# Kernel tuning notes

Measured on AMD Instinct MI355X. Metric: run time of the kernel, lower is better.

Reference implementation:

```python
import jax, jax.numpy as jnp
import numpy as np

H_HEADS = 8
TOP_K = 32


def _interp_matrix(n_out, n_in):
    # 1D linear-interp matrix matching torch trilinear, align_corners=False
    c = (jnp.arange(n_out, dtype=jnp.float32) + 0.5) * (n_in / n_out) - 0.5
    c = jnp.clip(c, 0.0, n_in - 1)
    i0 = jnp.floor(c).astype(jnp.int32)
    i1 = jnp.minimum(i0 + 1, n_in - 1)
    w = c - i0.astype(jnp.float32)
    r = jnp.arange(n_out)
    Mt = jnp.zeros((n_out, n_in), jnp.float32)
    return Mt.at[r, i0].add(1.0 - w).at[r, i1].add(w)


def _ln(x, g, b, eps=1e-5):
    m = x.mean(axis=-1, keepdims=True)
    v = ((x - m) ** 2).mean(axis=-1, keepdims=True)
    return (x - m) * jax.lax.rsqrt(v + eps) * g + b


def _forward(x, mask, pe, Wqkv, bqkv, Wo, bo, ln1_g, ln1_b, W1, b1, W2, b2,
             ln2_g, ln2_b, gate, mem_k, mem_v, fc1_w, fc1_b, fc2_w, fc2_b):
    B, D = x.shape[0], x.shape[1]
    H, HD, K = H_HEADS, D // H_HEADS, TOP_K
    # FeatureConcatenator treated as identity (x already concatenated features)
    Im = _interp_matrix(8, mask.shape[2])  # separable trilinear resize 64->8
    m8 = jnp.einsum('ai,bj,ck,nqijk->nqabc', Im, Im, Im, mask)
    h = x * m8 + pe  # masked features + learned absolute 3D positional enc
    tok = h.reshape(B, D, -1).transpose(0, 2, 1)  # [B, S=512, D]
    scale = 1.0 / jnp.sqrt(jnp.float32(HD))
    L = Wqkv.shape[0]
    for l in range(L):
        qkv = tok @ Wqkv[l] + bqkv[l]
        q, k, v = jnp.split(qkv, 3, axis=-1)
        hd = lambda t: t.reshape(B, -1, H, HD).transpose(0, 2, 1, 3)  # [B,H,S,d]
        q, k, v = hd(q), hd(k), hd(v)
        attn = jax.nn.softmax(jnp.einsum('bhsd,bhtd->bhst', q, k) * scale, axis=-1)
        out = jnp.einsum('bhst,bhtd->bhsd', attn, v)
        if l == 0:  # KNN memory layer: irregular top-k retrieval over memory bank
            sim = jnp.einsum('bhsd,bmd->bhsm', q, mem_k) * scale  # [B,H,S,M]
            top_sim, top_idx = jax.lax.top_k(sim, K)  # [B,H,S,K]
            mv = jnp.take_along_axis(mem_v[:, None, None], top_idx[..., None], axis=3)
            mem_out = jnp.einsum('bhsk,bhskd->bhsd', jax.nn.softmax(top_sim, axis=-1), mv)
            g = jax.nn.sigmoid(gate)[None, :, None, None]
            out = out * (1.0 - g) + mem_out * g
        out = out.transpose(0, 2, 1, 3).reshape(B, -1, D)
        tok = _ln(tok + out @ Wo[l] + bo[l], ln1_g[l], ln1_b[l])
        ff = jax.nn.gelu(tok @ W1[l] + b1[l], approximate=False) @ W2[l] + b2[l]
        tok = _ln(tok + ff, ln2_g[l], ln2_b[l])
    pooled = tok.mean(axis=1)  # global avg pool over all 512 voxels
    return jax.nn.gelu(pooled @ fc1_w + fc1_b, approximate=False) @ fc2_w + fc2_b


def setup_inputs() -> dict:
    key = jax.random.key(0)
    ks = jax.random.split(key, 24)
    B, D, Sp, M, L = 4, 512, 8, 8192, 6
    H, HD, FF, MLP, NC = 8, 64, 2048, 1024, 117
    nrm = lambda k, shp, s=0.02: jax.random.normal(k, shp, jnp.float32) * s
    return {
        'x': jax.random.normal(ks[0], (B, D, Sp, Sp, Sp), jnp.float32),
        'mask': jax.random.uniform(ks[1], (B, 1, 64, 64, 64), jnp.float32),
        'pe': nrm(ks[2], (1, D, Sp, Sp, Sp)),
        'Wqkv': nrm(ks[3], (L, D, 3 * D)),
        'bqkv': jnp.zeros((L, 3 * D), jnp.float32),
        'Wo': nrm(ks[4], (L, D, D)),
        'bo': jnp.zeros((L, D), jnp.float32),
        'ln1_g': jnp.ones((L, D), jnp.float32),
        'ln1_b': jnp.zeros((L, D), jnp.float32),
        'W1': nrm(ks[5], (L, D, FF)),
        'b1': jnp.zeros((L, FF), jnp.float32),
        'W2': nrm(ks[6], (L, FF, D)),
        'b2': jnp.zeros((L, D), jnp.float32),
        'ln2_g': jnp.ones((L, D), jnp.float32),
        'ln2_b': jnp.zeros((L, D), jnp.float32),
        'gate': jnp.zeros((H,), jnp.float32),
        'mem_k': jax.random.normal(ks[7], (B, M, HD), jnp.float32),
        'mem_v': jax.random.normal(ks[8], (B, M, HD), jnp.float32),
        'fc1_w': nrm(ks[9], (D, MLP)),
        'fc1_b': jnp.zeros((MLP,), jnp.float32),
        'fc2_w': nrm(ks[10], (MLP, NC)),
        'fc2_b': jnp.zeros((NC,), jnp.float32),
    }


def reference(x, mask, pe, Wqkv, bqkv, Wo, bo, ln1_g, ln1_b, W1, b1, W2, b2,
              ln2_g, ln2_b, gate, mem_k, mem_v, fc1_w, fc1_b, fc2_w, fc2_b):
    return _forward(x, mask, pe, Wqkv, bqkv, Wo, bo, ln1_g, ln1_b, W1, b1, W2,
                    b2, ln2_g, ln2_b, gate, mem_k, mem_v, fc1_w, fc1_b, fc2_w, fc2_b)
```

## Files before the change

kernel.cpp:

```cpp
#include <hip/hip_runtime.h>
#include <hip/hip_bf16.h>
#include <float.h>
#include <math.h>

#define NB 4
#define ND 512
#define NS 512
#define NH 8
#define NHD 64
#define NM 8192
#define NL 6
#define NFF 2048
#define NMLP 1024
#define NC 117

#define KCC 64
#define NCC (NM / KCC)
#define CAPB 160
#define TRIG 96

#define CAPS 352
#define TRIGS 96

#define AS1 __attribute__((address_space(1)))
// ... 515 lines not shown
            }
#pragma unroll
            for (int fm = 0; fm < FM; ++fm)
#pragma unroll
                for (int fn = 0; fn < FN; ++fn) {
                    acc[fm][fn] = __builtin_amdgcn_mfma_f32_16x16x32_bf16(fah[fm], fbh[fn], acc[fm][fn], 0, 0, 0);
                    acc[fm][fn] = __builtin_amdgcn_mfma_f32_16x16x32_bf16(fah[fm], fbl[fn], acc[fm][fn], 0, 0, 0);
                    acc[fm][fn] = __builtin_amdgcn_mfma_f32_16x16x32_bf16(fal[fm], fbh[fn], acc[fm][fn], 0, 0, 0);
                }
        }
    }
#pragma unroll
    for (int fm = 0; fm < FM; ++fm) {
#pragma unroll
        for (int fn = 0; fn < FN; ++fn) {
            int n = bn + wc * (BN / 2) + fn * 16 + (lane & 15);
            float bb = 0.f;
            if (EPI != 3) bb = bias[n];
#pragma unroll
            for (int r = 0; r < 4; ++r) {
                int m = bm + wr * (BM / 2) + fm * 16 + (lane >> 4) * 4 + r;
                float o = acc[fm][fn][r] + bb;
                if (EPI == 4) {
                    o = gelu_f(o);
                    ushort hh, ll;
                    split1(o, hh, ll);
                    size_t byb = (size_t)m * 2 * N + (size_t)(n >> 6) * 128 +
                                 (size_t)(((((n >> 3) & 7) * 16)) ^ ((m & 7) << 4)) + (n & 7) * 2;
                    *(ushort*)((char*)CH + byb) = hh;
                    *(ushort*)((char*)CL + byb) = ll;
                } else if (EPI == 5) {
                    int seg = n >> 9;
                    int hh_ = (n >> 6) & 7, dd = n & 63;
                    int bq = m >> 9, sq = m & 511;
                    ushort hh, ll;
                    if (seg == 0) {
                        split1(o * 0.125f, hh, ll);
                        size_t rr = (size_t)bq * 4096 + hh_ * 512 + sq;
                        size_t by = rr * 128 + (size_t)((((dd >> 3) * 16)) ^ ((sq & 7) << 4)) + (dd & 7) * 2;
                        *(ushort*)((char*)CH + by) = hh;
                        *(ushort*)((char*)CL + by) = ll;
                    } else if (seg == 1) {
                        split1(o, hh, ll);
                        size_t rr = (size_t)bq * 4096 + hh_ * 512 + sq;
                        size_t by = rr * 128 + (size_t)((((dd >> 3) * 16)) ^ ((sq & 7) << 4)) + (dd & 7) * 2;
                        *(ushort*)((char*)C2H + by) = hh;
                        *(ushort*)((char*)C2L + by) = ll;
                    } else {
                        split1(o, hh, ll);
                        size_t rr = (size_t)(bq * 8 + hh_) * 64 + dd;
                        size_t by = rr * 1024 + (size_t)(sq >> 6) * 128 +
                                    (size_t)(((((sq >> 3) & 7) * 16)) ^ ((dd & 7) << 4)) + (sq & 7) * 2;
                        *(ushort*)((char*)C3H + by) = hh;
                        *(ushort*)((char*)C3L + by) = ll;
                    }
                } else {
                    if (EPI == 1) o = gelu_f(o);
                    else if (EPI == 2) o += resid[(size_t)m * N + n];
                    C[(size_t)m * N + n] = o;
                }
            }
        }
    }
}

__global__ __launch_bounds__(256) void k_attn2(
    const ushort* __restrict__ QH, const ushort* __restrict__ QL,
    const ushort* __restrict__ KH, const ushort* __restrict__ KL,
    const ushort* __restrict__ VTH, const ushort* __restrict__ VTL,
    float* __restrict__ ao) {
    __shared__ __align__(16) char SM[81920];
    int qt = blockIdx.x, h = blockIdx.y, b = blockIdx.z;
    int tid = threadIdx.x, lane = tid & 63, wvi = tid >> 6;
    size_t R = ((size_t)(b * NH + h)) * NS;
    const char* KHg = (const char*)KH + R * 128;
    const char* KLg = (const char*)KL + R * 128;
    const char* VHg = (const char*)VTH + ((size_t)(b * NH + h) * 64) * 1024;
    const char* VLg = (const char*)VTL + ((size_t)(b * NH + h) * 64) * 1024;

    stage_lin((const char*)QH + (R + qt * 64) * 128, SM + 65536, wvi, lane);
    stage_lin((const char*)QL + (R + qt * 64) * 128, SM + 73728, wvi, lane);
    stage_lin(KHg, SM + 0, wvi, lane);
    stage_lin(KLg, SM + 8192, wvi, lane);
    stage_vt(VHg, 0, SM + 32768, wvi, lane);
    stage_vt(VLg, 0, SM + 40960, wvi, lane);
    __syncthreads();

    s16x8 fqh[2], fql[2];
#pragma unroll
    for (int ks = 0; ks < 2; ++ks) {
        int row = wvi * 16 + (lane & 15);
        int by = row * 128 + ((((ks * 32 + (lane >> 4) * 8) * 2)) ^ ((row & 7) << 4));
        fqh[ks] = *(const s16x8*)(SM + 65536 + by);
        fql[ks] = *(const s16x8*)(SM + 73728 + by);
    }

    float mr_[4] = {-FLT_MAX, -FLT_MAX, -FLT_MAX, -FLT_MAX};
    float lr_[4] = {0.f, 0.f, 0.f, 0.f};
    f32x4 acc_o[4] = {};

    for (int c = 0; c < 8; ++c) {
        const char* khc = SM + ((c & 1) ? 16384 : 0);
        const char* klc = khc + 8192;
        const char* vhc = SM + 32768 + ((c & 1) ? 16384 : 0);
        const char* vlc = vhc + 8192;
        if (c + 1 < 8) {
            char* khn = SM + ((c & 1) ? 0 : 16384);
            char* vhn = SM + 32768 + ((c & 1) ? 0 : 16384);
            stage_lin(KHg + (size_t)(c + 1) * 8192, khn, wvi, lane);
            stage_lin(KLg + (size_t)(c + 1) * 8192, khn + 8192, wvi, lane);
            stage_vt(VHg, (c + 1) * 128, vhn, wvi, lane);
            stage_vt(VLg, (c + 1) * 128, vhn + 8192, wvi, lane);
        }
        f32x4 sa[4] = {};
#pragma unroll
        for (int ks = 0; ks < 2; ++ks) {
            int kbyte = (ks * 32 + (lane >> 4) * 8) * 2;
#pragma unroll
            for (int fk = 0; fk < 4; ++fk) {
                int krow = fk * 16 + (lane & 15);
                int by = krow * 128 + (kbyte ^ ((krow & 7) << 4));
                s16x8 kh8 = *(const s16x8*)(khc + by);
                s16x8 kl8 = *(const s16x8*)(klc + by);
                sa[fk] = __builtin_amdgcn_mfma_f32_16x16x32_bf16(fqh[ks], kh8, sa[fk], 0, 0, 0);
                sa[fk] = __builtin_amdgcn_mfma_f32_16x16x32_bf16(fqh[ks], kl8, sa[fk], 0, 0, 0);
                sa[fk] = __builtin_amdgcn_mfma_f32_16x16x32_bf16(fql[ks], kh8, sa[fk], 0, 0, 0);
            }
        }
#pragma unroll
        for (int r = 0; r < 4; ++r) {
            float smax = fmaxf(fmaxf(sa[0][r], sa[1][r]), fmaxf(sa[2][r], sa[3][r]));
            smax = fmaxf(smax, __shfl_xor(smax, 1));
            smax = fmaxf(smax, __shfl_xor(smax, 2));
            smax = fmaxf(smax, __shfl_xor(smax, 4));
            smax = fmaxf(smax, __shfl_xor(smax, 8));
            float mn = fmaxf(mr_[r], smax);
            float alpha = __expf(mr_[r] - mn);
            mr_[r] = mn;
            float p0 = __expf(sa[0][r] - mn);
            float p1 = __expf(sa[1][r] - mn);
            float p2 = __expf(sa[2][r] - mn);
            float p3 = __expf(sa[3][r] - mn);
            float ls = p0 + p1 + p2 + p3;
            ls += __shfl_xor(ls, 1);
            ls += __shfl_xor(ls, 2);
            ls += __shfl_xor(ls, 4);
            ls += __shfl_xor(ls, 8);
            lr_[r] = lr_[r] * alpha + ls;
#pragma unroll
            for (int fd = 0; fd < 4; ++fd) acc_o[fd][r] *= alpha;
            int prow = wvi * 16 + (lane >> 4) * 4 + r;
            int sw = (prow & 7) << 4;
            int l15 = lane & 15;
            int wb = (l15 & 7) * 2;
            float pv_[4] = {p0, p1, p2, p3};
#pragma unroll
            for (int fk = 0; fk < 4; ++fk) {
                ushort hh, ll;
                split1(pv_[fk], hh, ll);
                int gran = fk * 2 + (l15 >> 3);
                int by = prow * 128 + ((gran * 16) ^ sw) + wb;
                *(ushort*)(SM + 65536 + by) = hh;
                *(ushort*)(SM + 73728 + by) = ll;
            }
        }
        s16x8 fph[2], fpl[2];
#pragma unroll
        for (int ks = 0; ks < 2; ++ks) {
            int prow = wvi * 16 + (lane & 15);
            int by = prow * 128 + ((((ks * 32 + (lane >> 4) * 8) * 2)) ^ ((prow & 7) << 4));
            fph[ks] = *(const s16x8*)(SM + 65536 + by);
            fpl[ks] = *(const s16x8*)(SM + 73728 + by);
        }
#pragma unroll
        for (int ks = 0; ks < 2; ++ks) {
            int kbyte = (ks * 32 + (lane >> 4) * 8) * 2;
#pragma unroll
            for (int fd = 0; fd < 4; ++fd) {
                int vrow = fd * 16 + (lane & 15);
                int by = vrow * 128 + (kbyte ^ ((vrow & 7) << 4));
                s16x8 vh8 = *(const s16x8*)(vhc + by);
                s16x8 vl8 = *(const s16x8*)(vlc + by);
                acc_o[fd] = __builtin_amdgcn_mfma_f32_16x16x32_bf16(fph[ks], vh8, acc_o[fd], 0, 0, 0);
                acc_o[fd] = __builtin_amdgcn_mfma_f32_16x16x32_bf16(fph[ks], vl8, acc_o[fd], 0, 0, 0);
                acc_o[fd] = __builtin_amdgcn_mfma_f32_16x16x32_bf16(fpl[ks], vh8, acc_o[fd], 0, 0, 0);
            }
        }
        __syncthreads();
    }
    float inv_[4];
#pragma unroll
    for (int r = 0; r < 4; ++r) inv_[r] = 1.0f / lr_[r];
#pragma unroll
    for (int fd = 0; fd < 4; ++fd)
#pragma unroll
        for (int r = 0; r < 4; ++r) {
            int srow = qt * 64 + wvi * 16 + (lane >> 4) * 4 + r;
            int col = h * 64 + fd * 16 + (lane & 15);
            ao[((size_t)(b * NS) + srow) * ND + col] = acc_o[fd][r] * inv_[r];
        }
}

__global__ __launch_bounds__(256) void k_attn(const float* __restrict__ qkv,
                                              float* __restrict__ ao) {
    __shared__ float qs[32][65];
    __shared__ float ks[64][65];
    __shared__ float sc[32][68];
    __shared__ float pm[32][8];
    __shared__ float Mrow[32], Srow[32], Arow[32];
    int s0 = blockIdx.x * 32, h = blockIdx.y, b = blockIdx.z;
    int tid = threadIdx.x, tx = tid & 15, ty = tid >> 4;
    const float* base = qkv + (size_t)b * NS * 1536;
#pragma unroll
    for (int i = 0; i < 8; ++i) {
        int idx = tid + i * 256;
        int r = idx >> 6, d = idx & 63;
        qs[r][d] = base[(size_t)(s0 + r) * 1536 + h * 64 + d] * 0.125f;
    }
    if (tid < 32) { Mrow[tid] = -FLT_MAX; Srow[tid] = 0.f; }
    float accp[2][4] = {};
    int rg = tid >> 3, gg = tid & 7;
    for (int c = 0; c < 8; ++c) {
        __syncthreads();
#pragma unroll
        for (int i = 0; i < 16; ++i) {
            int idx = tid + i * 256;
            int r = idx >> 6, d = idx & 63;
            ks[r][d] = base[(size_t)(c * 64 + r) * 1536 + 512 + h * 64 + d];
        }
        __syncthreads();
        float a00 = 0, a01 = 0, a02 = 0, a03 = 0, a10 = 0, a11 = 0, a12 = 0, a13 = 0;
#pragma unroll 8
        for (int d = 0; d < 64; ++d) {
            float q0 = qs[ty][d], q1 = qs[ty + 16][d];
            float k0 = ks[tx][d], k1 = ks[tx + 16][d], k2 = ks[tx + 32][d], k3 = ks[tx + 48][d];
            a00 += q0 * k0; a01 += q0 * k1; a02 += q0 * k2; a03 += q0 * k3;
            a10 += q1 * k0; a11 += q1 * k1; a12 += q1 * k2; a13 += q1 * k3;
        }
        sc[ty][tx] = a00; sc[ty][tx + 16] = a01; sc[ty][tx + 32] = a02; sc[ty][tx + 48] = a03;
        sc[ty + 16][tx] = a10; sc[ty + 16][tx + 16] = a11; sc[ty + 16][tx + 32] = a12; sc[ty + 16][tx + 48] = a13;
        __syncthreads();
        float lm = -FLT_MAX;
#pragma unroll
        for (int j = 0; j < 8; ++j) lm = fmaxf(lm, sc[rg][gg * 8 + j]);
        pm[rg][gg] = lm;
        __syncthreads();
        if (gg == 0) {
            float nm = Mrow[rg];
#pragma unroll
            for (int j = 0; j < 8; ++j) nm = fmaxf(nm, pm[rg][j]);
            Arow[rg] = __expf(Mrow[rg] - nm);
            Mrow[rg] = nm;
        }
        __syncthreads();
        float mr = Mrow[rg];
        float ssp = 0.f;
#pragma unroll
        for (int j = 0; j < 8; ++j) {
            float e = __expf(sc[rg][gg * 8 + j] - mr);
            sc[rg][gg * 8 + j] = e;
            ssp += e;
        }
        pm[rg][gg] = ssp;
        __syncthreads();
        if (gg == 0) {
            float s2 = 0.f;
#pragma unroll
            for (int j = 0; j < 8; ++j) s2 += pm[rg][j];
            Srow[rg] = Srow[rg] * Arow[rg] + s2;
        }
        float al0 = Arow[ty], al1 = Arow[ty + 16];
#pragma unroll
        for (int j = 0; j < 4; ++j) { accp[0][j] *= al0; accp[1][j] *= al1; }
        __syncthreads();
#pragma unroll
        for (int i = 0; i < 16; ++i) {
            int idx = tid + i * 256;
            int r = idx >> 6, d = idx & 63;
            ks[r][d] = base[(size_t)(c * 64 + r) * 1536 + 1024 + h * 64 + d];
        }
        __syncthreads();
#pragma unroll 8
        for (int kk = 0; kk < 64; ++kk) {
            float p0 = sc[ty][kk], p1 = sc[ty + 16][kk];
            float v0 = ks[kk][tx], v1 = ks[kk][tx + 16], v2 = ks[kk][tx + 32], v3 = ks[kk][tx + 48];
            accp[0][0] += p0 * v0; accp[0][1] += p0 * v1; accp[0][2] += p0 * v2; accp[0][3] += p0 * v3;
            accp[1][0] += p1 * v0; accp[1][1] += p1 * v1; accp[1][2] += p1 * v2; accp[1][3] += p1 * v3;
        }
    }
    __syncthreads();
    float inv0 = 1.0f / Srow[ty], inv1 = 1.0f / Srow[ty + 16];
    size_t o0 = ((size_t)(b * NS) + s0 + ty) * ND + h * 64;
    size_t o1 = ((size_t)(b * NS) + s0 + ty + 16) * ND + h * 64;
    ao[o0 + tx] = accp[0][0] * inv0;
    ao[o0 + tx + 16] = accp[0][1] * inv0;
    ao[o0 + tx + 32] = accp[0][2] * inv0;
    ao[o0 + tx + 48] = accp[0][3] * inv0;
    ao[o1 + tx] = accp[1][0] * inv1;
    ao[o1 + tx + 16] = accp[1][1] * inv1;
    ao[o1 + tx + 32] = accp[1][2] * inv1;
    ao[o1 + tx + 48] = accp[1][3] * inv1;
}

__global__ __launch_bounds__(256) void k_ksel(
    const float* __restrict__ sims, const float* __restrict__ mv,
    const float* __restrict__ gate, float* __restrict__ ao, int b) {
    __shared__ float bval[4][CAPS];
    __shared__ ushort bidx[4][CAPS];
    int tid = threadIdx.x, lane = tid & 63, wvi = tid >> 6;
    int gq = blockIdx.x * 2 + (wvi >> 1);
    int bb, q;
    if (b < 0) { bb = gq >> 12; q = gq & 4095; }
    else { bb = b; q = gq; }
    int hf = wvi & 1;
    const float* sr = sims + (size_t)gq * NM + hf * 4096;
    float* bv = &bval[wvi][0];
    ushort* bi = &bidx[wvi][0];
    unsigned long long lm = (1ULL << lane) - 1;
    {
        float4 v = *(const float4*)(sr + lane * 4);
        int m0 = lane * 4;
        int gI = hf * 4096 + m0;
        bv[m0 + 0] = v.x; bi[m0 + 0] = (ushort)(gI + 0);
        bv[m0 + 1] = v.y; bi[m0 + 1] = (ushort)(gI + 1);
        bv[m0 + 2] = v.z; bi[m0 + 2] = (ushort)(gI + 2);
        bv[m0 + 3] = v.w; bi[m0 + 3] = (ushort)(gI + 3);
    }
    float thr = shrink6v(bv, bi, 256, lane);
    int cnt = 32;
    float4 vA = *(const float4*)(sr + 256 + lane * 4);
    float4 vB = *(const float4*)(sr + 512 + lane * 4);
    for (int i = 1; i < 16; ++i) {
        float4 vC = vB;
        if (i + 2 < 16) vC = *(const float4*)(sr + (size_t)(i + 2) * 256 + lane * 4);
        int m0 = hf * 4096 + i * 256 + lane * 4;
        bool px = vA.x >= thr, py = vA.y >= thr, pz = vA.z >= thr, pw = vA.w >= thr;
        unsigned long long bx = __ballot(px), by = __ballot(py), bz = __ballot(pz), bw = __ballot(pw);
        int nx = (int)__popcll(bx), ny = (int)__popcll(by), nz = (int)__popcll(bz), nw = (int)__popcll(bw);
        int b0 = cnt, b1 = b0 + nx, b2 = b1 + ny, b3 = b2 + nz;
        if (px) { int p = b0 + (int)__popcll(bx & lm); bv[p] = vA.x; bi[p] = (ushort)(m0 + 0); }
        if (py) { int p = b1 + (int)__popcll(by & lm); bv[p] = vA.y; bi[p] = (ushort)(m0 + 1); }
        if (pz) { int p = b2 + (int)__popcll(bz & lm); bv[p] = vA.z; bi[p] = (ushort)(m0 + 2); }
        if (pw) { int p = b3 + (int)__popcll(bw & lm); bv[p] = vA.w; bi[p] = (ushort)(m0 + 3); }
        cnt = b3 + nw;
        if (cnt >= TRIGS) {
            thr = shrink6v(bv, bi, cnt, lane);
            cnt = 32;
        }
        vA = vB;
        vB = vC;
    }
    thr = shrink6v(bv, bi, cnt, lane);
    __syncthreads();

    if (hf == 0) {
        float mval;
        ushort midx;
        if (lane < 32) { mval = bval[wvi][lane]; midx = bidx[wvi][lane]; }
        else { mval = bval[wvi + 1][lane - 32]; midx = bidx[wvi + 1][lane - 32]; }
        unsigned long long k = packkey(mval, (int)midx);
        unsigned long long K = 0;
#pragma unroll 1
        for (int bit = 44; bit >= 0; --bit) {
            unsigned long long cand = K | (1ULL << bit);
            if ((int)__popcll(__ballot(k >= cand)) >= 32) K = cand;
        }
        unsigned long long m = __ballot(k >= K);
        if (k >= K) {
            int p = (int)__popcll(m & lm);
            bv[p] = mval;
            bi[p] = midx;
        }
        float val = (lane < 32) ? bv[lane] : -FLT_MAX;
        float mx = val;
#pragma unroll
        for (int off = 32; off; off >>= 1) mx = fmaxf(mx, __shfl_xor(mx, off));
        float e = (lane < 32) ? __expf(val - mx) : 0.f;
        float ssum = e;
#pragma unroll
        for (int off = 32; off; off >>= 1) ssum += __shfl_xor(ssum, off);
        float w = e / ssum;
        if (lane < 32) bv[lane] = w;
        float acc = 0.f;
        const float* vb = mv + (size_t)bb * NM * NHD;
#pragma unroll 4
        for (int j = 0; j < 32; ++j) {
            float ww = bv[j];
            int idx = (int)bi[j];
            acc += ww * vb[(size_t)idx * NHD + lane];
        }
        int h = q >> 9, s = q & 511;
        float g = 1.0f / (1.0f + __expf(-gate[h]));
        float* aop = ao + ((size_t)(bb * NS) + s) * ND + h * 64 + lane;
        *aop = *aop * (1.0f - g) + acc * g;
    }
}

__global__ __launch_bounds__(256, 2) void k_knn5(
    const float* __restrict__ qkv, const ushort* __restrict__ mkh,
    const ushort* __restrict__ mkl, const float* __restrict__ mv,
    const float* __restrict__ gate, float* __restrict__ ao) {
    __shared__ __align__(16) char SM[63760];
    ushort* kh0 = (ushort*)SM;
    ushort* kl0 = (ushort*)(SM + 8192);
    ushort* kh1 = (ushort*)(SM + 16384);
    ushort* kl1 = (ushort*)(SM + 24576);
    float* cval = (float*)(SM + 32768);
    ushort* cidx = (ushort*)(SM + 53248);
    float* thrV = (float*)(SM + 63488);
    int* cnt = (int*)(SM + 63616);
    int* sflag = (int*)(SM + 63744);
    ushort* qh = (ushort*)(SM + 32768);
    ushort* ql = (ushort*)(SM + 36864);
    int b = blockIdx.y, s0 = blockIdx.x * 4;
    int tid = threadIdx.x, lane = tid & 63, wvi = tid >> 6;
    const ushort* mhb = mkh + (size_t)b * NM * 64;
    const ushort* mlb = mkl + (size_t)b * NM * 64;
    {
        int q = tid >> 3, dbase = (tid & 7) * 8;
        const float* src = &qkv[((size_t)(b * NS) + s0 + (q & 3)) * 1536 + (q >> 2) * 64 + dbase];
        float v[8];
#pragma unroll
        for (int j = 0; j < 8; ++j) v[j] = src[j] * 0.125f;
        s16x8 hv, lv;
        split8(v, hv, lv);
        int by = q * 128 + ((dbase * 2) ^ ((q & 7) << 4));
        *(s16x8*)((char*)qh + by) = hv;
        *(s16x8*)((char*)ql + by) = lv;
    }
    stage_dma64(mhb, mlb, kh0, kl0, wvi, lane);
    __syncthreads();
    s16x8 fqh[2][2], fql[2][2];
#pragma unroll
    for (int fq = 0; fq < 2; ++fq)
#pragma unroll
        for (int ks = 0; ks < 2; ++ks) {
            int row = fq * 16 + (lane & 15);
            int kb2 = (ks * 32 + (lane >> 4) * 8) * 2;
            int by = row * 128 + (kb2 ^ ((row & 7) << 4));
            fqh[fq][ks] = *(const s16x8*)((const char*)qh + by);
            fql[fq][ks] = *(const s16x8*)((const char*)ql + by);
        }
    if (tid < 32) { cnt[tid] = 0; thrV[tid] = -FLT_MAX; }
    if (tid == 0) *sflag = 0;
    __syncthreads();
    int qbase4 = (lane >> 4) * 4;
    int mrow = (lane & 15);
    for (int c = 0; c < NCC; ++c) {
        ushort* khc = (c & 1) ? kh1 : kh0;
        ushort* klc = (c & 1) ? kl1 : kl0;
        if (c + 1 < NCC) {
            size_t ro = (size_t)(c + 1) * KCC * 64;
            stage_dma64(mhb + ro, mlb + ro, (c & 1) ? kh0 : kh1, (c & 1) ? kl0 : kl1, wvi, lane);
        }
        float thc[2][4];
#pragma unroll
        for (int fq = 0; fq < 2; ++fq)
#pragma unroll
            for (int r = 0; r < 4; ++r) thc[fq][r] = thrV[fq * 16 + qbase4 + r];
        f32x4 acc[2] = {};
#pragma unroll
        for (int ks = 0; ks < 2; ++ks) {
            int row = wvi * 16 + mrow;
            int kb2 = (ks * 32 + (lane >> 4) * 8) * 2;
            int by = row * 128 + (kb2 ^ ((row & 7) << 4));
            s16x8 kh8 = *(const s16x8*)((const char*)khc + by);
            s16x8 kl8 = *(const s16x8*)((const char*)klc + by);
#pragma unroll
            for (int fq = 0; fq < 2; ++fq) {
                acc[fq] = __builtin_amdgcn_mfma_f32_16x16x32_bf16(fqh[fq][ks], kh8, acc[fq], 0, 0, 0);
                acc[fq] = __builtin_amdgcn_mfma_f32_16x16x32_bf16(fqh[fq][ks], kl8, acc[fq], 0, 0, 0);
                acc[fq] = __builtin_amdgcn_mfma_f32_16x16x32_bf16(fql[fq][ks], kh8, acc[fq], 0, 0, 0);
            }
        }
#pragma unroll
        for (int fq = 0; fq < 2; ++fq)
#pragma unroll
            for (int r = 0; r < 4; ++r) {
                float v = acc[fq][r];
                if (v >= thc[fq][r]) {
                    int q = fq * 16 + qbase4 + r;
                    int pos = atomicAdd(&cnt[q], 1);
                    if (pos < CAPB) {
                        cval[q * CAPB + pos] = v;
                        cidx[q * CAPB + pos] = (ushort)(c * KCC + wvi * 16 + mrow);
                    }
                    if (pos == TRIG) *sflag = 1;
                }
            }
        __syncthreads();
        if (*sflag) {
#pragma unroll 1
            for (int qq = 0; qq < 8; ++qq) {
                int q = wvi * 8 + qq;
                shrink_cheap(cval, cidx, q, cnt[q], lane, &thrV[q]);
                if (lane == 0) cnt[q] = 32;
            }
            if (tid == 0) *sflag = 0;
            __syncthreads();
        }
    }
#pragma unroll 1
    for (int qq = 0; qq < 8; ++qq) {
        int q = wvi * 8 + qq;
        shrink_cheap(cval, cidx, q, cnt[q], lane, nullptr);
    }
    __syncthreads();
    if (tid < 32) {
        int q = tid;
        float mx = -FLT_MAX;
#pragma unroll
        for (int j = 0; j < 32; ++j) mx = fmaxf(mx, cval[q * CAPB + j]);
        float es[32];
        float ssum = 0.f;
#pragma unroll
        for (int j = 0; j < 32; ++j) { es[j] = __expf(cval[q * CAPB + j] - mx); ssum += es[j]; }
        float inv = 1.0f / ssum;
#pragma unroll
        for (int j = 0; j < 32; ++j) cval[q * CAPB + j] = es[j] * inv;
    }
    __syncthreads();
    {
        int q = tid >> 3, dseg = (tid & 7) * 8;
        int h = q >> 2, si = q & 3;
        float r0x = 0, r0y = 0, r0z = 0, r0w = 0, r1x = 0, r1y = 0, r1z = 0, r1w = 0;
        const float* vb = mv + (size_t)b * NM * NHD;
        for (int j = 0; j < 32; ++j) {
            float w = cval[q * CAPB + j];
            int idx = (int)cidx[q * CAPB + j];
            const float* row = vb + (size_t)idx * NHD + dseg;
            float4 v0 = *(const float4*)(row);
            float4 v1 = *(const float4*)(row + 4);
            r0x += w * v0.x; r0y += w * v0.y; r0z += w * v0.z; r0w += w * v0.w;
            r1x += w * v1.x; r1y += w * v1.y; r1z += w * v1.z; r1w += w * v1.w;
        }
        float g = 1.0f / (1.0f + __expf(-gate[h]));
        float omg = 1.0f - g;
        float* aop = ao + ((size_t)(b * NS) + s0 + si) * ND + h * 64 + dseg;
        float rr[8] = {r0x, r0y, r0z, r0w, r1x, r1y, r1z, r1w};
#pragma unroll
        for (int k = 0; k < 8; ++k) aop[k] = aop[k] * omg + rr[k] * g;
    }
}

__global__ __launch_bounds__(256) void k_ln(const float* __restrict__ X,
                                            const float* __restrict__ gam,
                                            const float* __restrict__ bet,
                                            float* __restrict__ Y) {
    __shared__ float red[4];
    __shared__ float sm, sv;
    int r = blockIdx.x, tid = threadIdx.x;
    const float* xr = X + (size_t)r * ND;
    float x0 = xr[tid], x1 = xr[tid + 256];
    float s = x0 + x1;
    for (int off = 32; off; off >>= 1) s += __shfl_down(s, off);
    if ((tid & 63) == 0) red[tid >> 6] = s;
    __syncthreads();
    if (tid == 0) sm = (red[0] + red[1] + red[2] + red[3]) * (1.0f / 512.0f);
    __syncthreads();
    float m = sm;
    float d0 = x0 - m, d1 = x1 - m;
    float vs = d0 * d0 + d1 * d1;
    for (int off = 32; off; off >>= 1) vs += __shfl_down(vs, off);
    if ((tid & 63) == 0) red[tid >> 6] = vs;
    __syncthreads();
    if (tid == 0) sv = rsqrtf((red[0] + red[1] + red[2] + red[3]) * (1.0f / 512.0f) + 1e-5f);
    __syncthreads();
    float rstd = sv;
    Y[(size_t)r * ND + tid] = d0 * rstd * gam[tid] + bet[tid];
    Y[(size_t)r * ND + tid + 256] = d1 * rstd * gam[tid + 256] + bet[tid + 256];
}

__global__ __launch_bounds__(256) void k_ln2(const float* __restrict__ X,
                                             const float* __restrict__ gam,
                                             const float* __restrict__ bet,
                                             float* __restrict__ Y,
                                             ushort* __restrict__ YH,
                                             ushort* __restrict__ YL) {
    __shared__ float red[4];
    __shared__ float sm, sv;
    int r = blockIdx.x, tid = threadIdx.x;
    const float* xr = X + (size_t)r * ND;
    float x0 = xr[tid], x1 = xr[tid + 256];
    float s = x0 + x1;
    for (int off = 32; off; off >>= 1) s += __shfl_down(s, off);
    if ((tid & 63) == 0) red[tid >> 6] = s;
    __syncthreads();
    if (tid == 0) sm = (red[0] + red[1] + red[2] + red[3]) * (1.0f / 512.0f);
    __syncthreads();
    float m = sm;
    float d0 = x0 - m, d1 = x1 - m;
    float vs = d0 * d0 + d1 * d1;
    for (int off = 32; off; off >>= 1) vs += __shfl_down(vs, off);
    if ((tid & 63) == 0) red[tid >> 6] = vs;
    __syncthreads();
    if (tid == 0) sv = rsqrtf((red[0] + red[1] + red[2] + red[3]) * (1.0f / 512.0f) + 1e-5f);
    __syncthreads();
    float rstd = sv;
    float y0 = d0 * rstd * gam[tid] + bet[tid];
    float y1 = d1 * rstd * gam[tid + 256] + bet[tid + 256];
    Y[(size_t)r * ND + tid] = y0;
    Y[(size_t)r * ND + tid + 256] = y1;
    int sw = (r & 7) << 4;
    char* oh = (char*)YH + (size_t)r * 1024;
    char* ol = (char*)YL + (size_t)r * 1024;
    ushort hh, ll;
    split1(y0, hh, ll);
    int k0 = tid;
    int by0 = (k0 >> 6) * 128 + ((((k0 >> 3) & 7) * 16) ^ sw) + (k0 & 7) * 2;
    *(ushort*)(oh + by0) = hh;
    *(ushort*)(ol + by0) = ll;
    split1(y1, hh, ll);
    int k1 = tid + 256;
    int by1 = (k1 >> 6) * 128 + ((((k1 >> 3) & 7) * 16) ^ sw) + (k1 & 7) * 2;
    *(ushort*)(oh + by1) = hh;
    *(ushort*)(ol + by1) = ll;
}

__global__ void k_pool2(const float* __restrict__ tok, float* __restrict__ part) {
    int c = blockIdx.x, b = blockIdx.y;
    int tid = threadIdx.x;
    int sp0 = c * 64;
    float a0 = 0.f, a1 = 0.f;
    const float* base = tok + ((size_t)(b * NS) + sp0) * ND;
#pragma unroll 4
    for (int i = 0; i < 64; ++i) {
        a0 += base[(size_t)i * ND + tid];
        a1 += base[(size_t)i * ND + tid + 256];
    }
    float* dst = part + ((size_t)(c * NB + b)) * ND;
    dst[tid] = a0;
    dst[tid + 256] = a1;
}

__global__ void k_pool3(const float* __restrict__ part, float* __restrict__ pooled) {
    int b = blockIdx.x, d = threadIdx.x;
    float s = 0.f;
#pragma unroll
    for (int c = 0; c < 8; ++c) s += part[((size_t)(c * NB + b)) * ND + d];
    pooled[b * ND + d] = s * (1.0f / 512.0f);
}

__global__ void k_fc1(const float* __restrict__ pooled, const float* __restrict__ w,
                      const float* __restrict__ bias, float* __restrict__ o1) {
    int id = blockIdx.x * 256 + threadIdx.x;
    int b = id >> 10, j = id & 1023;
    float acc = bias[j];
    for (int d = 0; d < ND; ++d) acc += pooled[b * ND + d] * w[(size_t)d * NMLP + j];
    o1[id] = gelu_f(acc);
}

__global__ __launch_bounds__(256) void k_fc2b(const float* __restrict__ o1,
                                              const float* __restrict__ w,
                                              const float* __restrict__ bias,
                                              float* __restrict__ out) {
    int c = blockIdx.x;
    int b = threadIdx.x >> 6, lane = threadIdx.x & 63;
    const float* o1b = o1 + b * NMLP;
    float acc = 0.f;
#pragma unroll
    for (int i = 0; i < 16; ++i) {
        int k = i * 64 + lane;
        acc += o1b[k] * w[(size_t)k * NC + c];
    }
    acc += __shfl_xor(acc, 32);
    acc += __shfl_xor(acc, 16);
    acc += __shfl_xor(acc, 8);
    acc += __shfl_xor(acc, 4);
    acc += __shfl_xor(acc, 2);
    acc += __shfl_xor(acc, 1);
    if (lane == 0) out[b * NC + c] = acc + bias[c];
}

extern "C" void kernel_launch(void* const* d_in, const int* in_sizes, int n_in,
                              void* d_out, int out_size, void* d_ws, size_t ws_size,
                              hipStream_t stream) {
    const float* x    = (const float*)d_in[0];
    const float* mask = (const float*)d_in[1];
    const float* pe   = (const float*)d_in[2];
    const float* Wqkv = (const float*)d_in[3];
    const float* bqkv = (const float*)d_in[4];
    const float* Wo   = (const float*)d_in[5];
    const float* bo   = (const float*)d_in[6];
    const float* ln1g = (const float*)d_in[7];
    const float* ln1b = (const float*)d_in[8];
    const float* W1   = (const float*)d_in[9];
    const float* b1   = (const float*)d_in[10];
    const float* W2   = (const float*)d_in[11];
    const float* b2   = (const float*)d_in[12];
    const float* ln2g = (const float*)d_in[13];
    const float* ln2b = (const float*)d_in[14];
    const float* gate = (const float*)d_in[15];
    const float* memk = (const float*)d_in[16];
    const float* memv = (const float*)d_in[17];
    const float* fc1w = (const float*)d_in[18];
    const float* fc1b = (const float*)d_in[19];
    const float* fc2w = (const float*)d_in[20];
    const float* fc2b_ = (const float*)d_in[21];
    float* out = (float*)d_out;

    float* ws = (float*)d_ws;

    float* m8     = ws;
    ushort* mkh   = (ushort*)(m8 + 2048);
    ushort* mkl   = mkh + 2097152;
    float* tok    = (float*)(mkl + 2097152);
    float* qkv    = tok + 1048576;
    float* ao     = qkv + 3145728;
    float* pooled = ao + 1048576;
    float* o1     = pooled + 2048;
    ushort* aH    = (ushort*)(o1 + 4096);
    ushort* aL    = aH + 1048576;
    ushort* WqTH  = aL + 1048576;
    ushort* WqTL  = WqTH + 4718592;
    ushort* WoTH  = WqTL + 4718592;
    ushort* WoTL  = WoTH + 1572864;
    ushort* W1TH  = WoTL + 1572864;
    ushort* W1TL  = W1TH + 6291456;
    ushort* W2TH  = W1TL + 6291456;
    ushort* W2TL  = W2TH + 6291456;
    float* simsb  = (float*)(W2TL + 6291456);
    ushort* fH  = (ushort*)(simsb + 4194304);
    ushort* fL  = fH + 4194304;
    float* ybuf = simsb + 8388608;
    float* ppart = simsb;
    ushort* QHb  = (ushort*)qkv;
    ushort* QLb  = QHb + 1048576;
    ushort* KHb  = QLb + 1048576;
    ushort* KLb  = KHb + 1048576;
    ushort* VTHb = KLb + 1048576;
    ushort* VTLb = VTHb + 1048576;

    size_t needNew = (size_t)((simsb + 33554432) - ws) * sizeof(float);
    size_t needBat = (size_t)((simsb + 134217728) - ws) * sizeof(float);

    if (ws_size >= needNew) {
        bool batched = ws_size >= needBat;
        k_m8<<<NB, 512, 0, stream>>>(mask, m8);
        k_mksplit<<<1024, 256, 0, stream>>>(memk, mkh, mkl);
        k_tok<<<dim3(16, 16, NB), dim3(32, 8), 0, stream>>>(x, pe, m8, tok);
        k_wsplitT<<<dim3(48, 8, 6), dim3(32, 8), 0, stream>>>(Wqkv, WqTH, WqTL, 512, 1536);
        k_wsplitT<<<dim3(16, 8, 6), dim3(32, 8), 0, stream>>>(Wo, WoTH, WoTL, 512, 512);
        k_wsplitT<<<dim3(64, 8, 6), dim3(32, 8), 0, stream>>>(W1, W1TH, W1TL, 512, 2048);
        k_wsplitT<<<dim3(16, 32, 6), dim3(32, 8), 0, stream>>>(W2, W2TH, W2TL, 2048, 512);
        k_asplit<<<512, 256, 0, stream>>>(tok, aH, aL, 512);

        for (int l = 0; l < NL; ++l) {
            k_gmm2<128, 128, 5><<<dim3(12, 16), 256, 0, stream>>>(
                aH, aL, WqTH + (size_t)l * 786432, WqTL + (size_t)l * 786432,
                bqkv + l * 1536, nullptr, nullptr, QHb, QLb, KHb, KLb, VTHb, VTLb,
                2048, 1536, 512, 0, 0, 0);
            k_attn2<<<dim3(8, NH, NB), 256, 0, stream>>>(QHb, QLb, KHb, KLb, VTHb, VTLb, ao);
            if (l == 0) {
                if (batched) {
                    k_gmm2<128, 128, 3><<<dim3(64, 32, NB), 256, 0, stream>>>(
                        QHb, QLb, mkh, mkl,
                        nullptr, nullptr, simsb, nullptr, nullptr, nullptr, nullptr,
                        nullptr, nullptr, 4096, 8192, 64,
                        262144, 524288, 33554432);
                    k_ksel<<<8192, 256, 0, stream>>>(simsb, memv, gate, ao, -1);
                } else {
                    for (int bb = 0; bb < NB; ++bb) {
                        k_gmm2<128, 128, 3><<<dim3(64, 32), 256, 0, stream>>>(
                            QHb + (size_t)bb * 262144, QLb + (size_t)bb * 262144,
                            mkh + (size_t)bb * 524288, mkl + (size_t)bb * 524288,
                            nullptr, nullptr, simsb, nullptr, nullptr, nullptr, nullptr,
                            nullptr, nullptr, 4096, 8192, 64, 0, 0, 0);
                        k_ksel<<<2048, 256, 0, stream>>>(simsb, memv, gate, ao, bb);
                    }
                }
            }
            k_asplit<<<512, 256, 0, stream>>>(ao, aH, aL, 512);
            k_gmm2<64, 64, 2><<<dim3(8, 32), 256, 0, stream>>>(
                aH, aL, WoTH + (size_t)l * 262144, WoTL + (size_t)l * 262144,
                bo + l * 512, tok, ybuf, nullptr, nullptr, nullptr, nullptr,
                nullptr, nullptr, 2048, 512, 512, 0, 0, 0);
            k_ln2<<<2048, 256, 0, stream>>>(ybuf, ln1g + l * 512, ln1b + l * 512, tok, aH, aL);
            k_gmm2<128, 128, 4><<<dim3(16, 16), 256, 0, stream>>>(
                aH, aL, W1TH + (size_t)l * 1048576, W1TL + (size_t)l * 1048576,
                b1 + l * 2048, nullptr, nullptr, fH, fL, nullptr, nullptr,
                nullptr, nullptr, 2048, 2048, 512, 0, 0, 0);
            k_gmm2<64, 64, 2><<<dim3(8, 32), 256, 0, stream>>>(
                fH, fL, W2TH + (size_t)l * 1048576, W2TL + (size_t)l * 1048576,
                b2 + l * 512, tok, ybuf, nullptr, nullptr, nullptr, nullptr,
                nullptr, nullptr, 2048, 512, 2048, 0, 0, 0);
            k_ln2<<<2048, 256, 0, stream>>>(ybuf, ln2g + l * 512, ln2b + l * 512, tok, aH, aL);
        }
        k_pool2<<<dim3(8, NB), 256, 0, stream>>>(tok, ppart);
        k_pool3<<<NB, 512, 0, stream>>>(ppart, pooled);
        k_fc1<<<16, 256, 0, stream>>>(pooled, fc1w, fc1b, o1);
        k_fc2b<<<NC, 256, 0, stream>>>(o1, fc2w, fc2b_, out);
        return;
    }

    float* m8b     = ws;
    ushort* mkh2   = (ushort*)(m8b + 2048);
    ushort* mkl2   = mkh2 + 2097152;
    float* tok2    = (float*)(mkl2 + 2097152);
    float* qkv2    = tok2 + 1048576;
    float* ao2     = qkv2 + 3145728;
    float* ybuf2   = ao2 + 1048576;
    float* ff12    = ybuf2 + 1048576;
    float* pooled2 = ff12 + 4194304;
    float* o12     = pooled2 + 2048;
    float* qmat2   = o12 + 4096;
    float* memkT2  = qmat2 + 1048576;
    float* simsb2  = memkT2 + 2097152;

    size_t needMid = (size_t)((simsb2 + 33554432) - ws) * sizeof(float);
    bool big = ws_size >= needMid;

    k_m8<<<NB, 512, 0, stream>>>(mask, m8b);
    if (big)
        k_memkT<<<dim3(NM / 32, 2, NB), dim3(32, 8), 0, stream>>>(memk, memkT2);
    else
        k_mksplit<<<1024, 256, 0, stream>>>(memk, mkh2, mkl2);
    k_tok<<<dim3(16, 16, NB), dim3(32, 8), 0, stream>>>(x, pe, m8b, tok2);

    for (int l = 0; l < NL; ++l) {
        k_gmm<128, 128, 0><<<dim3(12, 16), 256, 0, stream>>>(
            tok2, Wqkv + (size_t)l * 512 * 1536, bqkv + l * 1536, nullptr, qkv2, 2048, 1536, 512);
        k_attn<<<dim3(16, NH, NB), 256, 0, stream>>>(qkv2, ao2);
        if (l == 0) {
            if (big) {
                k_qmat<<<1024, 256, 0, stream>>>(qkv2, qmat2);
                for (int bb = 0; bb < NB; ++bb) {
                    k_gmm<128, 128, 3><<<dim3(64, 32), 256, 0, stream>>>(
                        qmat2 + (size_t)bb * 262144, memkT2 + (size_t)bb * 524288,
                        nullptr, nullptr, simsb2, 4096, 8192, 64);
                    k_ksel<<<2048, 256, 0, stream>>>(simsb2, memv, gate, ao2, bb);
                }
            } else {
                k_knn5<<<dim3(NS / 4, NB), 256, 0, stream>>>(qkv2, mkh2, mkl2, memv, gate, ao2);
            }
        }
        k_gmm<64, 64, 2><<<dim3(8, 32), 256, 0, stream>>>(
            ao2, Wo + (size_t)l * 512 * 512, bo + l * 512, tok2, ybuf2, 2048, 512, 512);
        k_ln<<<2048, 256, 0, stream>>>(ybuf2, ln1g + l * 512, ln1b + l * 512, tok2);
        k_gmm<128, 128, 1><<<dim3(16, 16), 256, 0, stream>>>(
            tok2, W1 + (size_t)l * 512 * 2048, b1 + l * 2048, nullptr, ff12, 2048, 2048, 512);
        k_gmm<64, 64, 2><<<dim3(8, 32), 256, 0, stream>>>(
            ff12, W2 + (size_t)l * 2048 * 512, b2 + l * 512, tok2, ybuf2, 2048, 512, 2048);
        k_ln<<<2048, 256, 0, stream>>>(ybuf2, ln2g + l * 512, ln2b + l * 512, tok2);
    }
    k_pool2<<<dim3(8, NB), 256, 0, stream>>>(tok2, simsb2);
    k_pool3<<<NB, 512, 0, stream>>>(simsb2, pooled2);
    k_fc1<<<16, 256, 0, stream>>>(pooled2, fc1w, fc1b, o12);
    k_fc2b<<<NC, 256, 0, stream>>>(o12, fc2w, fc2b_, out);
}
```

Measured before the change: 1.333 ms.

## Split KNN top-k selection across four waves per query with chunked batching

The top-k selection kernel now gives each query a whole 256-thread block, with each of the four waves scanning a 2048-entry quarter of the 8192 similarities instead of two waves per 4096 half. The final merge combines four candidate lists of 32 using dual ballots. The host also picks a batch chunk size of 1, 2 or 4 depending on workspace size rather than all-or-nothing batching. This shortens each wave's serial scan and raises parallelism, at the cost of twice as many blocks and a slightly costlier merge.

```diff
diff --git a/kernel.cpp b/kernel.cpp
--- a/kernel.cpp
+++ b/kernel.cpp
@@ -841,25 +841,23 @@
     ao[o1 + tx + 48] = accp[1][3] * inv1;
 }
 
-__global__ __launch_bounds__(256) void k_ksel(
+__global__ __launch_bounds__(256) void k_ksel4(
     const float* __restrict__ sims, const float* __restrict__ mv,
-    const float* __restrict__ gate, float* __restrict__ ao, int b) {
+    const float* __restrict__ gate, float* __restrict__ ao, int bbase) {
     __shared__ float bval[4][CAPS];
     __shared__ ushort bidx[4][CAPS];
     int tid = threadIdx.x, lane = tid & 63, wvi = tid >> 6;
-    int gq = blockIdx.x * 2 + (wvi >> 1);
-    int bb, q;
-    if (b < 0) { bb = gq >> 12; q = gq & 4095; }
-    else { bb = b; q = gq; }
-    int hf = wvi & 1;
-    const float* sr = sims + (size_t)gq * NM + hf * 4096;
+    int gq = blockIdx.x;
+    int bb = bbase + (gq >> 12), q = gq & 4095;
+    const float* sr = sims + (size_t)gq * NM + wvi * 2048;
     float* bv = &bval[wvi][0];
     ushort* bi = &bidx[wvi][0];
     unsigned long long lm = (1ULL << lane) - 1;
+
     {
         float4 v = *(const float4*)(sr + lane * 4);
         int m0 = lane * 4;
-        int gI = hf * 4096 + m0;
+        int gI = wvi * 2048 + m0;
         bv[m0 + 0] = v.x; bi[m0 + 0] = (ushort)(gI + 0);
         bv[m0 + 1] = v.y; bi[m0 + 1] = (ushort)(gI + 1);
         bv[m0 + 2] = v.z; bi[m0 + 2] = (ushort)(gI + 2);
@@ -867,12 +865,13 @@
     }
     float thr = shrink6v(bv, bi, 256, lane);
     int cnt = 32;
+
     float4 vA = *(const float4*)(sr + 256 + lane * 4);
     float4 vB = *(const float4*)(sr + 512 + lane * 4);
-    for (int i = 1; i < 16; ++i) {
+    for (int i = 1; i < 8; ++i) {
         float4 vC = vB;
-        if (i + 2 < 16) vC = *(const float4*)(sr + (size_t)(i + 2) * 256 + lane * 4);
-        int m0 = hf * 4096 + i * 256 + lane * 4;
+        if (i + 2 < 8) vC = *(const float4*)(sr + (size_t)(i + 2) * 256 + lane * 4);
+        int m0 = wvi * 2048 + i * 256 + lane * 4;
         bool px = vA.x >= thr, py = vA.y >= thr, pz = vA.z >= thr, pw = vA.w >= thr;
         unsigned long long bx = __ballot(px), by = __ballot(py), bz = __ballot(pz), bw = __ballot(pw);
         int nx = (int)__popcll(bx), ny = (int)__popcll(by), nz = (int)__popcll(bz), nw = (int)__popcll(bw);
@@ -892,23 +891,29 @@
     thr = shrink6v(bv, bi, cnt, lane);
     __syncthreads();
 
-    if (hf == 0) {
-        float mval;
-        ushort midx;
-        if (lane < 32) { mval = bval[wvi][lane]; midx = bidx[wvi][lane]; }
-        else { mval = bval[wvi + 1][lane - 32]; midx = bidx[wvi + 1][lane - 32]; }
-        unsigned long long k = packkey(mval, (int)midx);
+    if (wvi == 0) {
+        float v0 = bval[lane >> 5][lane & 31];
+        ushort i0 = bidx[lane >> 5][lane & 31];
+        float v1 = bval[2 + (lane >> 5)][lane & 31];
+        ushort i1 = bidx[2 + (lane >> 5)][lane & 31];
+        unsigned long long k0 = packkey(v0, (int)i0);
+        unsigned long long k1 = packkey(v1, (int)i1);
         unsigned long long K = 0;
 #pragma unroll 1
         for (int bit = 44; bit >= 0; --bit) {
             unsigned long long cand = K | (1ULL << bit);
-            if ((int)__popcll(__ballot(k >= cand)) >= 32) K = cand;
-        }
-        unsigned long long m = __ballot(k >= K);
-        if (k >= K) {
-            int p = (int)__popcll(m & lm);
-            bv[p] = mval;
-            bi[p] = midx;
+            int c = (int)__popcll(__ballot(k0 >= cand)) + (int)__popcll(__ballot(k1 >= cand));
+            if (c >= 32) K = cand;
+        }
+        int base = 0;
+        {
+            unsigned long long m = __ballot(k0 >= K);
+            if (k0 >= K) { int p = (int)__popcll(m & lm); bv[p] = v0; bi[p] = i0; }
+            base = (int)__popcll(m);
+        }
+        {
+            unsigned long long m = __ballot(k1 >= K);
+            if (k1 >= K) { int p = base + (int)__popcll(m & lm); bv[p] = v1; bi[p] = i1; }
         }
         float val = (lane < 32) ? bv[lane] : -FLT_MAX;
         float mx = val;
@@ -1271,10 +1276,11 @@
     ushort* VTLb = VTHb + 1048576;
 
     size_t needNew = (size_t)((simsb + 33554432) - ws) * sizeof(float);
-    size_t needBat = (size_t)((simsb + 134217728) - ws) * sizeof(float);
+    size_t need2   = needNew + (size_t)33554432 * sizeof(float);
+    size_t need4   = needNew + (size_t)3 * 33554432 * sizeof(float);
 
     if (ws_size >= needNew) {
-        bool batched = ws_size >= needBat;
+        int cb = (ws_size >= need4) ? 4 : ((ws_size >= need2) ? 2 : 1);
         k_m8<<<NB, 512, 0, stream>>>(mask, m8);
         k_mksplit<<<1024, 256, 0, stream>>>(memk, mkh, mkl);
         k_tok<<<dim3(16, 16, NB), dim3(32, 8), 0, stream>>>(x, pe, m8, tok);
@@ -1291,22 +1297,14 @@
                 2048, 1536, 512, 0, 0, 0);
             k_attn2<<<dim3(8, NH, NB), 256, 0, stream>>>(QHb, QLb, KHb, KLb, VTHb, VTLb, ao);
             if (l == 0) {
-                if (batched) {
-                    k_gmm2<128, 128, 3><<<dim3(64, 32, NB), 256, 0, stream>>>(
-                        QHb, QLb, mkh, mkl,
+                for (int bb0 = 0; bb0 < NB; bb0 += cb) {
+                    k_gmm2<128, 128, 3><<<dim3(64, 32, cb), 256, 0, stream>>>(
+                        QHb + (size_t)bb0 * 262144, QLb + (size_t)bb0 * 262144,
+                        mkh + (size_t)bb0 * 524288, mkl + (size_t)bb0 * 524288,
                         nullptr, nullptr, simsb, nullptr, nullptr, nullptr, nullptr,
                         nullptr, nullptr, 4096, 8192, 64,
                         262144, 524288, 33554432);
-                    k_ksel<<<8192, 256, 0, stream>>>(simsb, memv, gate, ao, -1);
-                } else {
-                    for (int bb = 0; bb < NB; ++bb) {
-                        k_gmm2<128, 128, 3><<<dim3(64, 32), 256, 0, stream>>>(
-                            QHb + (size_t)bb * 262144, QLb + (size_t)bb * 262144,
-                            mkh + (size_t)bb * 524288, mkl + (size_t)bb * 524288,
-                            nullptr, nullptr, simsb, nullptr, nullptr, nullptr, nullptr,
-                            nullptr, nullptr, 4096, 8192, 64, 0, 0, 0);
-                        k_ksel<<<2048, 256, 0, stream>>>(simsb, memv, gate, ao, bb);
-                    }
+                    k_ksel4<<<4096 * cb, 256, 0, stream>>>(simsb, memv, gate, ao, bb0);
                 }
             }
             k_asplit<<<512, 256, 0, stream>>>(ao, aH, aL, 512);
@@ -1367,7 +1365,7 @@
                     k_gmm<128, 128, 3><<<dim3(64, 32), 256, 0, stream>>>(
                         qmat2 + (size_t)bb * 262144, memkT2 + (size_t)bb * 524288,
                         nullptr, nullptr, simsb2, 4096, 8192, 64);
-                    k_ksel<<<2048, 256, 0, stream>>>(simsb2, memv, gate, ao2, bb);
+                    k_ksel4<<<4096, 256, 0, stream>>>(simsb2, memv, gate, ao2, bb);
                 }
             } else {
                 k_knn5<<<dim3(NS / 4, NB), 256, 0, stream>>>(qkv2, mkh2, mkl2, memv, gate, ao2);
```

Result: slower. 1.383 ms (+3.8%).
